# Performance work log

Measured on AMD Instinct MI355X. Metric: run time of the kernel, lower is better.

Reference implementation:

```python
import jax, jax.numpy as jnp
import numpy as np

LAMBDA = 1.0          # lambda_param
SIGMA = 1.0           # RBF bandwidth (sigkernel convention: exp(-||x-y||^2 / sigma))
DYADIC_ORDER = 2
F = 2 ** DYADIC_ORDER # dyadic refinement factor per time axis

B, M_POP, DIM, SEQ_LEN = 4, 16, 8, 65


def _rbf_gram(X, Y):
    # X: (m, L, d), Y: (n, L, d) -> static kernel Gram (m, n, L, L)
    sx = jnp.sum(X * X, -1)                       # (m, L)
    sy = jnp.sum(Y * Y, -1)                       # (n, L)
    inner = jnp.einsum('isd,jtd->ijst', X, Y)     # (m, n, L, L)
    d2 = sx[:, None, :, None] + sy[None, :, None, :] - 2.0 * inner
    return jnp.exp(-d2 / SIGMA)


def _increments(G):
    # double increment of the static Gram over time, then dyadic refinement
    inc = G[..., 1:, 1:] + G[..., :-1, :-1] - G[..., 1:, :-1] - G[..., :-1, 1:]
    inc = jnp.repeat(jnp.repeat(inc, F, axis=-2), F, axis=-1) / (F * F)
    return inc  # (..., S, S) with S = F*(L-1)


def _solve_pde(M):
    # Goursat PDE explicit finite-difference scheme (as in sigkernel):
    # K[i+1,j+1] = (K[i+1,j]+K[i,j+1])*(1 + m/2 + m^2/12) - K[i,j]*(1 - m^2/12)
    dtype = M.dtype
    S = M.shape[0]

    def row_step(prev_row, m_row):
        def cell(k_left, inp):
            k00, k01, m = inp
            a = 1.0 + 0.5 * m + m * m * (1.0 / 12.0)
            b = 1.0 - m * m * (1.0 / 12.0)
            k_new = (k_left + k01) * a - k00 * b
            return k_new, k_new
        _, tail = jax.lax.scan(cell, jnp.asarray(1.0, dtype),
                               (prev_row[:-1], prev_row[1:], m_row))
        new_row = jnp.concatenate([jnp.ones((1,), dtype), tail])
        return new_row, None

    row0 = jnp.ones((S + 1,), dtype)
    last_row, _ = jax.lax.scan(row_step, row0, M)
    return last_row[-1]


def _gram_sig(X, Y):
    # signature kernel Gram matrix: X (m,L,d), Y (n,L,d) -> (m,n)
    Minc = _increments(_rbf_gram(X, Y))
    return jax.vmap(jax.vmap(_solve_pde))(Minc)


def setup_inputs() -> dict:
    key = jax.random.key(0)
    k1, k2 = jax.random.split(key)
    generated_samples = jax.random.normal(k1, (B, M_POP, DIM, SEQ_LEN), dtype=jnp.float32)
    real_sample = jax.random.normal(k2, (B, DIM, SEQ_LEN), dtype=jnp.float32)
    return {"generated_samples": generated_samples, "real_sample": real_sample}


def reference(generated_samples, real_sample):
    # generated_samples: (B, m, dim, L); real_sample: (B, dim, L)
    gen = jnp.swapaxes(generated_samples, -1, -2)          # (B, m, L, d)
    real = jnp.swapaxes(real_sample, -1, -2)[:, None]      # (B, 1, L, d)
    m = gen.shape[1]
    K_XX = jax.vmap(_gram_sig)(gen, gen)                   # (B, m, m)
    K_XY = jax.vmap(_gram_sig)(gen, real)                  # (B, m, 1)
    self_sim = (jnp.sum(K_XX, axis=(-1, -2))
                - jnp.trace(K_XX, axis1=-2, axis2=-1)) / (m * (m - 1))
    cross_sim = jnp.mean(K_XY, axis=(-1, -2))
    return jnp.mean(LAMBDA / 2.0 * self_sim - cross_sim)
```

## Files before the change

kernel.cpp:

```cpp
#include <hip/hip_runtime.h>


#define SEQ   65
#define DIMS  8
#define MPOP  16
#define NBATCH 4
#define NPAIR_XX 120
#define NBLOCKS (NBATCH*(NPAIR_XX + MPOP))
#define MST 67

__device__ __forceinline__ float wave_shr1(float x) {
    int xi = __builtin_bit_cast(int, x);
    int r  = __builtin_amdgcn_update_dpp(xi, xi, 0x138 , 0xF, 0xF, false);
    return __builtin_bit_cast(float, r);
}

__global__ __launch_bounds__(64) void sigker_dpp_kernel(
    const float* __restrict__ gen,
    const float* __restrict__ realp,
    float* __restrict__ out)
{
    __shared__ float YsL[SEQ][DIMS];
    __shared__ float MmL[64 * MST];

    const int tid = threadIdx.x;
    const int bid = blockIdx.x;
    const int I   = tid;

    int b, ii, jj; bool cross;
    if (bid < NBATCH * NPAIR_XX) {
        b = bid / NPAIR_XX;
        int p = bid % NPAIR_XX;
        int i = 0, acc = 0;
        while (p >= acc + (MPOP - 1 - i)) { acc += (MPOP - 1 - i); ++i; }
        ii = i; jj = i + 1 + (p - acc); cross = false;
    } else {
        int t = bid - NBATCH * NPAIR_XX;
        b = t / MPOP; ii = t % MPOP; jj = 0; cross = true;
    }

    const float* Xg = gen + (size_t)(b * MPOP + ii) * (DIMS * SEQ);
    const float* Yg = cross ? (realp + (size_t)b * (DIMS * SEQ))
                            : (gen + (size_t)(b * MPOP + jj) * (DIMS * SEQ));

    for (int f = tid; f < SEQ * DIMS; f += 64) {
        int d = f / SEQ, s = f - d * SEQ;
        YsL[s][d] = Yg[f];
    }
    float x0[DIMS], x1[DIMS];
    #pragma unroll
    for (int d = 0; d < DIMS; ++d) {
        x0[d] = Xg[d * SEQ + I];
        x1[d] = Xg[d * SEQ + I + 1];
    }
    __syncthreads();

    float e0p, e1p;
    {
        float d0 = 0.f, d1 = 0.f;
        #pragma unroll
        for (int d = 0; d < DIMS; ++d) {
            float y = YsL[0][d];
            float a0 = x0[d] - y; d0 += a0 * a0;
            float a1 = x1[d] - y; d1 += a1 * a1;
        }
        e0p = __expf(-d0); e1p = __expf(-d1);
    }
    float* mrow = &MmL[I * MST];
    for (int t = 1; t < SEQ; ++t) {
        float d0 = 0.f, d1 = 0.f;
        #pragma unroll
        for (int d = 0; d < DIMS; ++d) {
            float y = YsL[t][d];
            float a0 = x0[d] - y; d0 += a0 * a0;
            float a1 = x1[d] - y; d1 += a1 * a1;
        }
        float e0 = __expf(-d0), e1 = __expf(-d1);
        mrow[t - 1] = (e1 + e0p - e1p - e0) * (1.0f / 16.0f);
        e0p = e0; e1p = e1;
    }

    float l0 = 1.f, l1 = 1.f, l2 = 1.f, l3 = 1.f;
    float b0 = 1.f, b1 = 1.f, b2 = 1.f, b3 = 1.f;
    float cnext = 1.f;
    float mnext = mrow[0];

    for (int DT = 0; DT < 127; ++DT) {
        float t0 = wave_shr1(b0);
        float t1 = wave_shr1(b1);
        float t2 = wave_shr1(b2);
        float t3 = wave_shr1(b3);
        float c = cnext; cnext = t3;
        if (I == 0) { t0 = t1 = t2 = t3 = 1.f; c = 1.f; }
        int J = DT - I;
        float m = mnext;
        int Jn = J + 1; Jn = Jn < 0 ? 0 : (Jn > 63 ? 63 : Jn);
        mnext = mrow[Jn];
        if (J >= 0 && J < 64) {
            if (J == 0) c = 1.f;
            float q12 = m * m * (1.0f / 12.0f);
            float a   = 1.0f + 0.5f * m + q12;
            float nb  = q12 - 1.0f;
            float u0 = a * t0 + nb * c;
            float u1 = a * t1 + nb * t0;
            float u2 = a * t2 + nb * t1;
            float u3 = a * t3 + nb * t2;
            float q1 = a * l0 + u0;
            float q2 = a * q1 + u1;
            float q3 = a * q2 + u2;
            float q4 = a * q3 + u3;
            u0 = a * q1 + nb * l0; u1 = a * q2 + nb * q1;
            u2 = a * q3 + nb * q2; u3 = a * q4 + nb * q3;
            float r1 = a * l1 + u0;
            float r2 = a * r1 + u1;
            float r3 = a * r2 + u2;
            float r4 = a * r3 + u3;
            u0 = a * r1 + nb * l1; u1 = a * r2 + nb * r1;
            u2 = a * r3 + nb * r2; u3 = a * r4 + nb * r3;
            float s1 = a * l2 + u0;
            float s2 = a * s1 + u1;
            float s3 = a * s2 + u2;
            float s4 = a * s3 + u3;
            u0 = a * s1 + nb * l2; u1 = a * s2 + nb * s1;
            u2 = a * s3 + nb * s2; u3 = a * s4 + nb * s3;
            float v1 = a * l3 + u0;
            float v2 = a * v1 + u1;
            float v3 = a * v2 + u2;
            float v4 = a * v3 + u3;
            b0 = v1; b1 = v2; b2 = v3; b3 = v4;
            l0 = q4; l1 = r4; l2 = s4; l3 = v4;
        }
    }

    if (tid == 63) {
        float w = cross ? (-1.0f / 32.0f) : (1.0f / 480.0f);
        atomicAdd(out, w * b3);
    }
}

extern "C" void kernel_launch(void* const* d_in, const int* in_sizes, int n_in,
                              void* d_out, int out_size, void* d_ws, size_t ws_size,
                              hipStream_t stream) {
    const float* gen   = (const float*)d_in[0];
    const float* realp = (const float*)d_in[1];
    if (n_in >= 2 && in_sizes[0] == NBATCH * DIMS * SEQ) {
        gen   = (const float*)d_in[1];
        realp = (const float*)d_in[0];
    }
    float* out = (float*)d_out;
    hipMemsetAsync(out, 0, sizeof(float), stream);
    sigker_dpp_kernel<<<NBLOCKS, 64, 0, stream>>>(gen, realp, out);
}
```

Before: 97.62 us.

## Split Gram increment computation across four waves and batch-prefetch PDE inputs

Launches 256 threads per block so four waves each compute a 16-step slice of the RBF increment rows into shared memory, then only the first wave runs the DPP wavefront PDE sweep. The anti-diagonal loop now runs 128 steps in groups of four, loading the next four m values from LDS ahead of use to hide LDS latency. This shortens the serial exp/distance prologue at the cost of extra idle waves per block during the PDE phase and an extra barrier.

```diff
diff --git a/kernel.cpp b/kernel.cpp
--- a/kernel.cpp
+++ b/kernel.cpp
@@ -15,7 +15,11 @@
     return __builtin_bit_cast(float, r);
 }
 
-__global__ __launch_bounds__(64) void sigker_dpp_kernel(
+__device__ __forceinline__ int clamp63(int v) {
+    return v < 0 ? 0 : (v > 63 ? 63 : v);
+}
+
+__global__ __launch_bounds__(256) void sigker_kernel(
     const float* __restrict__ gen,
     const float* __restrict__ realp,
     float* __restrict__ out)
@@ -24,8 +28,9 @@
     __shared__ float MmL[64 * MST];
 
     const int tid = threadIdx.x;
+    const int I   = tid & 63;
+    const int c   = tid >> 6;
     const int bid = blockIdx.x;
-    const int I   = tid;
 
     int b, ii, jj; bool cross;
     if (bid < NBATCH * NPAIR_XX) {
@@ -43,7 +48,7 @@
     const float* Yg = cross ? (realp + (size_t)b * (DIMS * SEQ))
                             : (gen + (size_t)(b * MPOP + jj) * (DIMS * SEQ));
 
-    for (int f = tid; f < SEQ * DIMS; f += 64) {
+    for (int f = tid; f < SEQ * DIMS; f += 256) {
         int d = f / SEQ, s = f - d * SEQ;
         YsL[s][d] = Yg[f];
     }
@@ -55,82 +60,105 @@
     }
     __syncthreads();
 
-    float e0p, e1p;
     {
-        float d0 = 0.f, d1 = 0.f;
+        float* mrow = &MmL[I * MST];
+        const int t0 = c * 16;
+        float e0p, e1p;
+        {
+            float d0 = 0.f, d1 = 0.f;
+            #pragma unroll
+            for (int d = 0; d < DIMS; ++d) {
+                float y = YsL[t0][d];
+                float a0 = x0[d] - y; d0 += a0 * a0;
+                float a1 = x1[d] - y; d1 += a1 * a1;
+            }
+            e0p = __expf(-d0); e1p = __expf(-d1);
+        }
         #pragma unroll
-        for (int d = 0; d < DIMS; ++d) {
-            float y = YsL[0][d];
-            float a0 = x0[d] - y; d0 += a0 * a0;
-            float a1 = x1[d] - y; d1 += a1 * a1;
+        for (int t = 1; t <= 16; ++t) {
+            float d0 = 0.f, d1 = 0.f;
+            #pragma unroll
+            for (int d = 0; d < DIMS; ++d) {
+                float y = YsL[t0 + t][d];
+                float a0 = x0[d] - y; d0 += a0 * a0;
+                float a1 = x1[d] - y; d1 += a1 * a1;
+            }
+            float e0 = __expf(-d0), e1 = __expf(-d1);
+            mrow[t0 + t - 1] = (e1 + e0p - e1p - e0) * (1.0f / 16.0f);
+            e0p = e0; e1p = e1;
         }
-        e0p = __expf(-d0); e1p = __expf(-d1);
     }
-    float* mrow = &MmL[I * MST];
-    for (int t = 1; t < SEQ; ++t) {
-        float d0 = 0.f, d1 = 0.f;
-        #pragma unroll
-        for (int d = 0; d < DIMS; ++d) {
-            float y = YsL[t][d];
-            float a0 = x0[d] - y; d0 += a0 * a0;
-            float a1 = x1[d] - y; d1 += a1 * a1;
-        }
-        float e0 = __expf(-d0), e1 = __expf(-d1);
-        mrow[t - 1] = (e1 + e0p - e1p - e0) * (1.0f / 16.0f);
-        e0p = e0; e1p = e1;
-    }
+    __syncthreads();
+    if (tid >= 64) return;
 
+    const float* mrow = &MmL[I * MST];
     float l0 = 1.f, l1 = 1.f, l2 = 1.f, l3 = 1.f;
     float b0 = 1.f, b1 = 1.f, b2 = 1.f, b3 = 1.f;
     float cnext = 1.f;
-    float mnext = mrow[0];
 
-    for (int DT = 0; DT < 127; ++DT) {
-        float t0 = wave_shr1(b0);
-        float t1 = wave_shr1(b1);
-        float t2 = wave_shr1(b2);
-        float t3 = wave_shr1(b3);
-        float c = cnext; cnext = t3;
-        if (I == 0) { t0 = t1 = t2 = t3 = 1.f; c = 1.f; }
-        int J = DT - I;
-        float m = mnext;
-        int Jn = J + 1; Jn = Jn < 0 ? 0 : (Jn > 63 ? 63 : Jn);
-        mnext = mrow[Jn];
-        if (J >= 0 && J < 64) {
-            if (J == 0) c = 1.f;
-            float q12 = m * m * (1.0f / 12.0f);
-            float a   = 1.0f + 0.5f * m + q12;
-            float nb  = q12 - 1.0f;
-            float u0 = a * t0 + nb * c;
-            float u1 = a * t1 + nb * t0;
-            float u2 = a * t2 + nb * t1;
-            float u3 = a * t3 + nb * t2;
-            float q1 = a * l0 + u0;
-            float q2 = a * q1 + u1;
-            float q3 = a * q2 + u2;
-            float q4 = a * q3 + u3;
-            u0 = a * q1 + nb * l0; u1 = a * q2 + nb * q1;
-            u2 = a * q3 + nb * q2; u3 = a * q4 + nb * q3;
-            float r1 = a * l1 + u0;
-            float r2 = a * r1 + u1;
-            float r3 = a * r2 + u2;
-            float r4 = a * r3 + u3;
-            u0 = a * r1 + nb * l1; u1 = a * r2 + nb * r1;
-            u2 = a * r3 + nb * r2; u3 = a * r4 + nb * r3;
-            float s1 = a * l2 + u0;
-            float s2 = a * s1 + u1;
-            float s3 = a * s2 + u2;
-            float s4 = a * s3 + u3;
-            u0 = a * s1 + nb * l2; u1 = a * s2 + nb * s1;
-            u2 = a * s3 + nb * s2; u3 = a * s4 + nb * s3;
-            float v1 = a * l3 + u0;
-            float v2 = a * v1 + u1;
-            float v3 = a * v2 + u2;
-            float v4 = a * v3 + u3;
-            b0 = v1; b1 = v2; b2 = v3; b3 = v4;
-            l0 = q4; l1 = r4; l2 = s4; l3 = v4;
-        }
+#define STEP(DTv, MV) do {                                              \
+        float t0_ = wave_shr1(b0);                                      \
+        float t1_ = wave_shr1(b1);                                      \
+        float t2_ = wave_shr1(b2);                                      \
+        float t3_ = wave_shr1(b3);                                      \
+        float cc_ = cnext; cnext = t3_;                                 \
+        if (I == 0) { t0_ = t1_ = t2_ = t3_ = 1.f; cc_ = 1.f; }         \
+        int J_ = (DTv) - I;                                             \
+        if ((unsigned)J_ < 64u) {                                       \
+            if (J_ == 0) cc_ = 1.f;                                     \
+            float m_   = (MV);                                          \
+            float q12_ = m_ * m_ * (1.0f / 12.0f);                      \
+            float a_   = 1.0f + 0.5f * m_ + q12_;                       \
+            float nb_  = q12_ - 1.0f;                                   \
+            float u0_ = a_ * t0_ + nb_ * cc_;                           \
+            float u1_ = a_ * t1_ + nb_ * t0_;                           \
+            float u2_ = a_ * t2_ + nb_ * t1_;                           \
+            float u3_ = a_ * t3_ + nb_ * t2_;                           \
+            float q1_ = a_ * l0 + u0_;                                  \
+            float q2_ = a_ * q1_ + u1_;                                 \
+            float q3_ = a_ * q2_ + u2_;                                 \
+            float q4_ = a_ * q3_ + u3_;                                 \
+            u0_ = a_ * q1_ + nb_ * l0;  u1_ = a_ * q2_ + nb_ * q1_;     \
+            u2_ = a_ * q3_ + nb_ * q2_; u3_ = a_ * q4_ + nb_ * q3_;     \
+            float r1_ = a_ * l1 + u0_;                                  \
+            float r2_ = a_ * r1_ + u1_;                                 \
+            float r3_ = a_ * r2_ + u2_;                                 \
+            float r4_ = a_ * r3_ + u3_;                                 \
+            u0_ = a_ * r1_ + nb_ * l1;  u1_ = a_ * r2_ + nb_ * r1_;     \
+            u2_ = a_ * r3_ + nb_ * r2_; u3_ = a_ * r4_ + nb_ * r3_;     \
+            float s1_ = a_ * l2 + u0_;                                  \
+            float s2_ = a_ * s1_ + u1_;                                 \
+            float s3_ = a_ * s2_ + u2_;                                 \
+            float s4_ = a_ * s3_ + u3_;                                 \
+            u0_ = a_ * s1_ + nb_ * l2;  u1_ = a_ * s2_ + nb_ * s1_;     \
+            u2_ = a_ * s3_ + nb_ * s2_; u3_ = a_ * s4_ + nb_ * s3_;     \
+            float v1_ = a_ * l3 + u0_;                                  \
+            float v2_ = a_ * v1_ + u1_;                                 \
+            float v3_ = a_ * v2_ + u2_;                                 \
+            float v4_ = a_ * v3_ + u3_;                                 \
+            b0 = v1_; b1 = v2_; b2 = v3_; b3 = v4_;                     \
+            l0 = q4_; l1 = r4_; l2 = s4_; l3 = v4_;                     \
+        }                                                               \
+    } while (0)
+
+    float m0 = mrow[clamp63(0 - I)];
+    float m1 = mrow[clamp63(1 - I)];
+    float m2 = mrow[clamp63(2 - I)];
+    float m3 = mrow[clamp63(3 - I)];
+
+    for (int g = 0; g < 32; ++g) {
+        const int DT0 = g * 4;
+        float n0 = mrow[clamp63(DT0 + 4 - I)];
+        float n1 = mrow[clamp63(DT0 + 5 - I)];
+        float n2 = mrow[clamp63(DT0 + 6 - I)];
+        float n3 = mrow[clamp63(DT0 + 7 - I)];
+        STEP(DT0 + 0, m0);
+        STEP(DT0 + 1, m1);
+        STEP(DT0 + 2, m2);
+        STEP(DT0 + 3, m3);
+        m0 = n0; m1 = n1; m2 = n2; m3 = n3;
     }
+#undef STEP
 
     if (tid == 63) {
         float w = cross ? (-1.0f / 32.0f) : (1.0f / 480.0f);
@@ -149,5 +177,5 @@
     }
     float* out = (float*)d_out;
     hipMemsetAsync(out, 0, sizeof(float), stream);
-    sigker_dpp_kernel<<<NBLOCKS, 64, 0, stream>>>(gen, realp, out);
+    sigker_kernel<<<NBLOCKS, 256, 0, stream>>>(gen, realp, out);
 }
```

Result: no change. 96.28 us (-1.4%).

## Process two kernel pairs per wave with interleaved PDE sweeps and padded boundaries

Applied to the files above, without the earlier changes.

Each 64-lane block now solves two independent signature-kernel PDEs, interleaving their diagonal sweeps so the two dependent FMA chains can hide each other's latency. Zero-padded increment rows remove the per-step J-range branch. The RBF Gram is computed via norms and dot products, with neighbour values exchanged by DPP shifts instead of recomputing distances. The atomic accumulation plus memset is replaced by per-pair workspace writes and a separate reduction kernel. This halves the number of blocks (272 down to 136) in exchange for more ILP per wave, and adds a second kernel launch.

```diff
diff --git a/kernel.cpp b/kernel.cpp
--- a/kernel.cpp
+++ b/kernel.cpp
@@ -6,136 +6,236 @@
 #define MPOP  16
 #define NBATCH 4
 #define NPAIR_XX 120
-#define NBLOCKS (NBATCH*(NPAIR_XX + MPOP))
-#define MST 67
+#define NPAIRS (NBATCH*(NPAIR_XX + MPOP))
+#define NBLK   (NPAIRS/2)
 
 __device__ __forceinline__ float wave_shr1(float x) {
     int xi = __builtin_bit_cast(int, x);
-    int r  = __builtin_amdgcn_update_dpp(xi, xi, 0x138 , 0xF, 0xF, false);
+    int r  = __builtin_amdgcn_update_dpp(xi, xi, 0x138, 0xF, 0xF, false);
     return __builtin_bit_cast(float, r);
 }
-
-__global__ __launch_bounds__(64) void sigker_dpp_kernel(
+__device__ __forceinline__ float wave_shl1(float x) {
+    int xi = __builtin_bit_cast(int, x);
+    int r  = __builtin_amdgcn_update_dpp(xi, xi, 0x130, 0xF, 0xF, false);
+    return __builtin_bit_cast(float, r);
+}
+__device__ __forceinline__ float ldm(const float* base, int idx) {
+    return base[idx < 0 ? 0 : idx];
+}
+
+struct PS { float l0,l1,l2,l3,b0,b1,b2,b3,cn; };
+
+__device__ __forceinline__ void pde_step(PS& s, float m, bool lane0) {
+    float t0 = wave_shr1(s.b0);
+    float t1 = wave_shr1(s.b1);
+    float t2 = wave_shr1(s.b2);
+    float t3 = wave_shr1(s.b3);
+    if (lane0) { t0 = 1.f; t1 = 1.f; t2 = 1.f; t3 = 1.f; }
+    float c = s.cn; s.cn = t3;
+    float q12 = m * m * (1.0f / 12.0f);
+    float a   = 1.0f + 0.5f * m + q12;
+    float nb  = q12 - 1.0f;
+    float u0 = a*t0 + nb*c;
+    float u1 = a*t1 + nb*t0;
+    float u2 = a*t2 + nb*t1;
+    float u3 = a*t3 + nb*t2;
+    float q1 = a*s.l0 + u0;
+    float q2 = a*q1 + u1;
+    float q3 = a*q2 + u2;
+    float q4 = a*q3 + u3;
+    u0 = a*q1 + nb*s.l0; u1 = a*q2 + nb*q1; u2 = a*q3 + nb*q2; u3 = a*q4 + nb*q3;
+    float r1 = a*s.l1 + u0;
+    float r2 = a*r1 + u1;
+    float r3 = a*r2 + u2;
+    float r4 = a*r3 + u3;
+    u0 = a*r1 + nb*s.l1; u1 = a*r2 + nb*r1; u2 = a*r3 + nb*r2; u3 = a*r4 + nb*r3;
+    float w1 = a*s.l2 + u0;
+    float w2 = a*w1 + u1;
+    float w3 = a*w2 + u2;
+    float w4 = a*w3 + u3;
+    u0 = a*w1 + nb*s.l2; u1 = a*w2 + nb*w1; u2 = a*w3 + nb*w2; u3 = a*w4 + nb*w3;
+    float v1 = a*s.l3 + u0;
+    float v2 = a*v1 + u1;
+    float v3 = a*v2 + u2;
+    float v4 = a*v3 + u3;
+    s.b0=v1; s.b1=v2; s.b2=v3; s.b3=v4;
+    s.l0=q4; s.l1=r4; s.l2=w4; s.l3=v4;
+}
+
+__device__ __forceinline__ void decode_pair(int p, int& b, int& ii, int& jj,
+                                            bool& cross) {
+    if (p < NBATCH * NPAIR_XX) {
+        b = p / NPAIR_XX;
+        int q = p % NPAIR_XX;
+        int i = 0, acc = 0;
+        while (q >= acc + (MPOP - 1 - i)) { acc += (MPOP - 1 - i); ++i; }
+        ii = i; jj = i + 1 + (q - acc); cross = false;
+    } else {
+        int t = p - NBATCH * NPAIR_XX;
+        b = t / MPOP; ii = t % MPOP; jj = 0; cross = true;
+    }
+}
+
+__global__ __launch_bounds__(64, 1) void sigker_kernel(
     const float* __restrict__ gen,
     const float* __restrict__ realp,
-    float* __restrict__ out)
+    float* __restrict__ ws)
 {
-    __shared__ float YsL[SEQ][DIMS];
-    __shared__ float MmL[64 * MST];
+    __shared__ __align__(16) float YsA[SEQ * DIMS], YsB[SEQ * DIMS];
+    __shared__ float YnA[SEQ], YnB[SEQ], R64A[SEQ], R64B[SEQ];
+    __shared__ float MmA[64 * 66], MmB[64 * 66];
 
     const int tid = threadIdx.x;
+    const int I   = tid;
+    const bool lane0 = (I == 0);
     const int bid = blockIdx.x;
-    const int I   = tid;
-
-    int b, ii, jj; bool cross;
-    if (bid < NBATCH * NPAIR_XX) {
-        b = bid / NPAIR_XX;
-        int p = bid % NPAIR_XX;
-        int i = 0, acc = 0;
-        while (p >= acc + (MPOP - 1 - i)) { acc += (MPOP - 1 - i); ++i; }
-        ii = i; jj = i + 1 + (p - acc); cross = false;
-    } else {
-        int t = bid - NBATCH * NPAIR_XX;
-        b = t / MPOP; ii = t % MPOP; jj = 0; cross = true;
-    }
-
-    const float* Xg = gen + (size_t)(b * MPOP + ii) * (DIMS * SEQ);
-    const float* Yg = cross ? (realp + (size_t)b * (DIMS * SEQ))
-                            : (gen + (size_t)(b * MPOP + jj) * (DIMS * SEQ));
-
+    const int pA = 2 * bid, pB = 2 * bid + 1;
+
+    int bA_, iA, jA; bool crA;  decode_pair(pA, bA_, iA, jA, crA);
+    int bB_, iB, jB; bool crB;  decode_pair(pB, bB_, iB, jB, crB);
+
+    const float* XgA = gen + (size_t)(bA_ * MPOP + iA) * (DIMS * SEQ);
+    const float* YgA = crA ? (realp + (size_t)bA_ * (DIMS * SEQ))
+                           : (gen + (size_t)(bA_ * MPOP + jA) * (DIMS * SEQ));
+    const float* XgB = gen + (size_t)(bB_ * MPOP + iB) * (DIMS * SEQ);
+    const float* YgB = crB ? (realp + (size_t)bB_ * (DIMS * SEQ))
+                           : (gen + (size_t)(bB_ * MPOP + jB) * (DIMS * SEQ));
+
+    MmA[66 * I] = 0.f;  MmA[66 * I + 65] = 0.f;
+    MmB[66 * I] = 0.f;  MmB[66 * I + 65] = 0.f;
     for (int f = tid; f < SEQ * DIMS; f += 64) {
         int d = f / SEQ, s = f - d * SEQ;
-        YsL[s][d] = Yg[f];
-    }
-    float x0[DIMS], x1[DIMS];
+        YsA[s * DIMS + d] = YgA[f];
+        YsB[s * DIMS + d] = YgB[f];
+    }
+    float xA[DIMS], x64A[DIMS], xB[DIMS], x64B[DIMS];
+    float xnA = 0.f, xn64A = 0.f, xnB = 0.f, xn64B = 0.f;
     #pragma unroll
     for (int d = 0; d < DIMS; ++d) {
-        x0[d] = Xg[d * SEQ + I];
-        x1[d] = Xg[d * SEQ + I + 1];
+        xA[d]   = XgA[d * SEQ + I];    xnA   += xA[d] * xA[d];
+        x64A[d] = XgA[d * SEQ + 64];   xn64A += x64A[d] * x64A[d];
+        xB[d]   = XgB[d * SEQ + I];    xnB   += xB[d] * xB[d];
+        x64B[d] = XgB[d * SEQ + 64];   xn64B += x64B[d] * x64B[d];
     }
     __syncthreads();
 
-    float e0p, e1p;
+    for (int t = tid; t < SEQ; t += 64) {
+        const float4* yv = (const float4*)&YsA[t * DIMS];
+        float4 ya = yv[0], yb = yv[1];
+        float yn  = ya.x*ya.x + ya.y*ya.y + ya.z*ya.z + ya.w*ya.w
+                  + yb.x*yb.x + yb.y*yb.y + yb.z*yb.z + yb.w*yb.w;
+        float dot = x64A[0]*ya.x + x64A[1]*ya.y + x64A[2]*ya.z + x64A[3]*ya.w
+                  + x64A[4]*yb.x + x64A[5]*yb.y + x64A[6]*yb.z + x64A[7]*yb.w;
+        YnA[t] = yn;
+        R64A[t] = __expf(2.f*dot - xn64A - yn);
+        const float4* zv = (const float4*)&YsB[t * DIMS];
+        float4 za = zv[0], zb = zv[1];
+        float zn  = za.x*za.x + za.y*za.y + za.z*za.z + za.w*za.w
+                  + zb.x*zb.x + zb.y*zb.y + zb.z*zb.z + zb.w*zb.w;
+        float dtB = x64B[0]*za.x + x64B[1]*za.y + x64B[2]*za.z + x64B[3]*za.w
+                  + x64B[4]*zb.x + x64B[5]*zb.y + x64B[6]*zb.z + x64B[7]*zb.w;
+        YnB[t] = zn;
+        R64B[t] = __expf(2.f*dtB - xn64B - zn);
+    }
+    __syncthreads();
+
+    float* mwA = &MmA[66 * I];
+    float* mwB = &MmB[66 * I];
+    float epA, enpA, epB, enpB;
     {
-        float d0 = 0.f, d1 = 0.f;
+        const float4* yv = (const float4*)&YsA[0];
+        float4 ya = yv[0], yb = yv[1];
+        float dA = xA[0]*ya.x + xA[1]*ya.y + xA[2]*ya.z + xA[3]*ya.w
+                 + xA[4]*yb.x + xA[5]*yb.y + xA[6]*yb.z + xA[7]*yb.w;
+        float eA = __expf(2.f*dA - xnA - YnA[0]);
+        float enA = wave_shl1(eA);
+        enA = (I == 63) ? R64A[0] : enA;
+        epA = eA; enpA = enA;
+        const float4* zv = (const float4*)&YsB[0];
+        float4 za = zv[0], zb = zv[1];
+        float dB = xB[0]*za.x + xB[1]*za.y + xB[2]*za.z + xB[3]*za.w
+                 + xB[4]*zb.x + xB[5]*zb.y + xB[6]*zb.z + xB[7]*zb.w;
+        float eB = __expf(2.f*dB - xnB - YnB[0]);
+        float enB = wave_shl1(eB);
+        enB = (I == 63) ? R64B[0] : enB;
+        epB = eB; enpB = enB;
+    }
+    #pragma unroll 4
+    for (int t = 1; t < SEQ; ++t) {
+        const float4* yv = (const float4*)&YsA[t * DIMS];
+        float4 ya = yv[0], yb = yv[1];
+        float dA = xA[0]*ya.x + xA[1]*ya.y + xA[2]*ya.z + xA[3]*ya.w
+                 + xA[4]*yb.x + xA[5]*yb.y + xA[6]*yb.z + xA[7]*yb.w;
+        float eA = __expf(2.f*dA - xnA - YnA[t]);
+        float enA = wave_shl1(eA);
+        enA = (I == 63) ? R64A[t] : enA;
+        mwA[t] = ((enA - enpA) + (epA - eA)) * (1.0f / 16.0f);
+        epA = eA; enpA = enA;
+        const float4* zv = (const float4*)&YsB[t * DIMS];
+        float4 za = zv[0], zb = zv[1];
+        float dB = xB[0]*za.x + xB[1]*za.y + xB[2]*za.z + xB[3]*za.w
+                 + xB[4]*zb.x + xB[5]*zb.y + xB[6]*zb.z + xB[7]*zb.w;
+        float eB = __expf(2.f*dB - xnB - YnB[t]);
+        float enB = wave_shl1(eB);
+        enB = (I == 63) ? R64B[t] : enB;
+        mwB[t] = ((enB - enpB) + (epB - eB)) * (1.0f / 16.0f);
+        epB = eB; enpB = enB;
+    }
+
+    PS SA = {1,1,1,1, 1,1,1,1, 1};
+    PS SB = {1,1,1,1, 1,1,1,1, 1};
+    const int ib = 1 - I;
+    const float* brA = &MmA[66 * I];
+    const float* brB = &MmB[66 * I];
+
+    float mA[8], mB[8];
+    #pragma unroll
+    for (int k = 0; k < 8; ++k) { mA[k] = ldm(brA, ib + k); mB[k] = ldm(brB, ib + k); }
+
+    for (int g = 0; g < 14; ++g) {
+        float nA[8], nB[8];
+        const int D8 = g * 8 + 8;
         #pragma unroll
-        for (int d = 0; d < DIMS; ++d) {
-            float y = YsL[0][d];
-            float a0 = x0[d] - y; d0 += a0 * a0;
-            float a1 = x1[d] - y; d1 += a1 * a1;
+        for (int k = 0; k < 8; ++k) {
+            nA[k] = ldm(brA, ib + D8 + k);
+            nB[k] = ldm(brB, ib + D8 + k);
         }
-        e0p = __expf(-d0); e1p = __expf(-d1);
-    }
-    float* mrow = &MmL[I * MST];
-    for (int t = 1; t < SEQ; ++t) {
-        float d0 = 0.f, d1 = 0.f;
         #pragma unroll
-        for (int d = 0; d < DIMS; ++d) {
-            float y = YsL[t][d];
-            float a0 = x0[d] - y; d0 += a0 * a0;
-            float a1 = x1[d] - y; d1 += a1 * a1;
+        for (int k = 0; k < 8; ++k) {
+            pde_step(SA, mA[k], lane0);
+            pde_step(SB, mB[k], lane0);
         }
-        float e0 = __expf(-d0), e1 = __expf(-d1);
-        mrow[t - 1] = (e1 + e0p - e1p - e0) * (1.0f / 16.0f);
-        e0p = e0; e1p = e1;
-    }
-
-    float l0 = 1.f, l1 = 1.f, l2 = 1.f, l3 = 1.f;
-    float b0 = 1.f, b1 = 1.f, b2 = 1.f, b3 = 1.f;
-    float cnext = 1.f;
-    float mnext = mrow[0];
-
-    for (int DT = 0; DT < 127; ++DT) {
-        float t0 = wave_shr1(b0);
-        float t1 = wave_shr1(b1);
-        float t2 = wave_shr1(b2);
-        float t3 = wave_shr1(b3);
-        float c = cnext; cnext = t3;
-        if (I == 0) { t0 = t1 = t2 = t3 = 1.f; c = 1.f; }
-        int J = DT - I;
-        float m = mnext;
-        int Jn = J + 1; Jn = Jn < 0 ? 0 : (Jn > 63 ? 63 : Jn);
-        mnext = mrow[Jn];
-        if (J >= 0 && J < 64) {
-            if (J == 0) c = 1.f;
-            float q12 = m * m * (1.0f / 12.0f);
-            float a   = 1.0f + 0.5f * m + q12;
-            float nb  = q12 - 1.0f;
-            float u0 = a * t0 + nb * c;
-            float u1 = a * t1 + nb * t0;
-            float u2 = a * t2 + nb * t1;
-            float u3 = a * t3 + nb * t2;
-            float q1 = a * l0 + u0;
-            float q2 = a * q1 + u1;
-            float q3 = a * q2 + u2;
-            float q4 = a * q3 + u3;
-            u0 = a * q1 + nb * l0; u1 = a * q2 + nb * q1;
-            u2 = a * q3 + nb * q2; u3 = a * q4 + nb * q3;
-            float r1 = a * l1 + u0;
-            float r2 = a * r1 + u1;
-            float r3 = a * r2 + u2;
-            float r4 = a * r3 + u3;
-            u0 = a * r1 + nb * l1; u1 = a * r2 + nb * r1;
-            u2 = a * r3 + nb * r2; u3 = a * r4 + nb * r3;
-            float s1 = a * l2 + u0;
-            float s2 = a * s1 + u1;
-            float s3 = a * s2 + u2;
-            float s4 = a * s3 + u3;
-            u0 = a * s1 + nb * l2; u1 = a * s2 + nb * s1;
-            u2 = a * s3 + nb * s2; u3 = a * s4 + nb * s3;
-            float v1 = a * l3 + u0;
-            float v2 = a * v1 + u1;
-            float v3 = a * v2 + u2;
-            float v4 = a * v3 + u3;
-            b0 = v1; b1 = v2; b2 = v3; b3 = v4;
-            l0 = q4; l1 = r4; l2 = s4; l3 = v4;
-        }
-    }
+        #pragma unroll
+        for (int k = 0; k < 8; ++k) { mA[k] = nA[k]; mB[k] = nB[k]; }
+    }
+    float eAt[7], eBt[7];
+    #pragma unroll
+    for (int k = 0; k < 7; ++k) {
+        eAt[k] = ldm(brA, ib + 120 + k);
+        eBt[k] = ldm(brB, ib + 120 + k);
+    }
+    #pragma unroll
+    for (int k = 0; k < 8; ++k) { pde_step(SA, mA[k], lane0); pde_step(SB, mB[k], lane0); }
+    #pragma unroll
+    for (int k = 0; k < 7; ++k) { pde_step(SA, eAt[k], lane0); pde_step(SB, eBt[k], lane0); }
 
     if (tid == 63) {
-        float w = cross ? (-1.0f / 32.0f) : (1.0f / 480.0f);
-        atomicAdd(out, w * b3);
-    }
+        float wA = crA ? (-1.0f / 32.0f) : (1.0f / 480.0f);
+        float wB = crB ? (-1.0f / 32.0f) : (1.0f / 480.0f);
+        ws[pA] = wA * SA.b3;
+        ws[pB] = wB * SB.b3;
+    }
+}
+
+__global__ __launch_bounds__(64, 1) void sigker_reduce(
+    const float* __restrict__ ws, float* __restrict__ out)
+{
+    const int lane = threadIdx.x;
+    float s = 0.f;
+    for (int k = lane; k < NPAIRS; k += 64) s += ws[k];
+    #pragma unroll
+    for (int off = 32; off >= 1; off >>= 1) s += __shfl_xor(s, off);
+    if (lane == 0) out[0] = s;
 }
 
 extern "C" void kernel_launch(void* const* d_in, const int* in_sizes, int n_in,
@@ -147,7 +247,8 @@
         gen   = (const float*)d_in[1];
         realp = (const float*)d_in[0];
     }
+    float* ws  = (float*)d_ws;
     float* out = (float*)d_out;
-    hipMemsetAsync(out, 0, sizeof(float), stream);
-    sigker_dpp_kernel<<<NBLOCKS, 64, 0, stream>>>(gen, realp, out);
-}
+    sigker_kernel<<<NBLK, 64, 0, stream>>>(gen, realp, ws);
+    sigker_reduce<<<1, 64, 0, stream>>>(ws, out);
+}
```

Result: slower. 103.3 us (+5.8%).
